# Optimization experiments

Hardware: AMD Instinct MI355X
Metric: run time of the kernel (lower is better)

## Reference

```python
import jax, jax.numpy as jnp
import numpy as np

B, L, K, D = 1024, 8, 16, 64
_KSCALE = 1.0 / np.sqrt(K * D)  # keep channel roughly norm-preserving over layers


def setup_inputs() -> dict:
    key = jax.random.key(0)
    k1, k2, k3, k4 = jax.random.split(key, 4)
    state_re = jax.random.normal(k1, (B, D, D), dtype=jnp.float32)
    state_im = jax.random.normal(k2, (B, D, D), dtype=jnp.float32)
    kraus_re = jax.random.normal(k3, (L, K, D, D), dtype=jnp.float32) * _KSCALE
    kraus_im = jax.random.normal(k4, (L, K, D, D), dtype=jnp.float32) * _KSCALE
    return {"state_re": state_re, "state_im": state_im,
            "kraus_re": kraus_re, "kraus_im": kraus_im}


def reference(state_re, state_im, kraus_re, kraus_im):
    # rho: [B, d, d] complex density matrices; kraus: [L, K, d, d]
    rho = (state_re + 1j * state_im).astype(jnp.complex64)
    kraus = (kraus_re + 1j * kraus_im).astype(jnp.complex64)

    def layer_step(rho, Kl):
        # Kl: [K, d, d]. output_state = sum_k  K_k @ rho @ K_k^dagger
        tmp = jnp.einsum('kij,bjl->kbil', Kl, rho)            # K_k @ rho
        rho_new = jnp.einsum('kbil,kml->bim', tmp, Kl.conj())  # (...) @ K_k^dagger, summed over k
        return rho_new, None

    rho, _ = jax.lax.scan(layer_step, rho, kraus)
    # return real/imag stacked as float32: [2, B, d, d]
    return jnp.stack([rho.real, rho.imag])
```

## Files before the change

kernel.cpp:

```cpp
#include <hip/hip_runtime.h>
#include <hip/hip_fp16.h>

#define D 64
#define NKR 16
#define NB 1024
#define NL 8
#define LSTR 72

typedef __attribute__((ext_vector_type(8))) _Float16 half8;
typedef __attribute__((ext_vector_type(4))) float f32x4;
typedef __attribute__((ext_vector_type(4))) int i32x4;

static __device__ __forceinline__ half8 neg8(half8 x) {
    i32x4 u = __builtin_bit_cast(i32x4, x);
    u = u ^ (int)0x80008000;
    return __builtin_bit_cast(half8, u);
}

union Pack4 { _Float16 h[4]; uint2 u; };

__global__ void kconv_kernel(const float* __restrict__ re, const float* __restrict__ im,
                             _Float16* __restrict__ out) {
    int plane = blockIdx.y;
    int idx = blockIdx.x * blockDim.x + threadIdx.x;
    const float* src = plane ? im : re;
    float4 v = ((const float4*)src)[idx];
    int e = idx * 4;
    int lk = e >> 12;
    int rem = e & 4095;
    Pack4 p;
    p.h[0] = (_Float16)v.x; p.h[1] = (_Float16)v.y;
    p.h[2] = (_Float16)v.z; p.h[3] = (_Float16)v.w;
    *(uint2*)(out + ((size_t)lk * 2 + plane) * 4096 + rem) = p.u;
}

__global__ void sconv_kernel(const float* __restrict__ re, const float* __restrict__ im,
                             _Float16* __restrict__ out) {
    __shared__ float tile[64][65];
    int b = blockIdx.x;
    int t = threadIdx.x;
    for (int plane = 0; plane < 2; ++plane) {
        const float* src = (plane ? im : re) + (size_t)b * 4096;
        __syncthreads();
        #pragma unroll
        for (int i = 0; i < 16; ++i) {
            int e = t + 256 * i;
            tile[e >> 6][e & 63] = src[e];
        }
        __syncthreads();
        _Float16* o = out + ((size_t)b * 2 + plane) * 4096;
        #pragma unroll
        for (int i = 0; i < 16; ++i) {
            int e = t + 256 * i;
            o[e] = (_Float16)tile[e & 63][e >> 6];
        }
    }
}

__global__ __launch_bounds__(256, 4) void layer_kernel(
    const _Float16* __restrict__ rho_in,
    _Float16* __restrict__ rho_out,
    float* __restrict__ final_out,
    const _Float16* __restrict__ kraus,
    int last)
{
    __shared__ __align__(16) _Float16 Klds[2][D][LSTR];
    __shared__ __align__(16) _Float16 Trow[2][D][LSTR];

    const int b    = blockIdx.x;
    const int t    = threadIdx.x;
    const int wv   = t >> 6;
    const int lane = t & 63;
    const int quad = lane >> 4;
    const int l15  = lane & 15;

    half8 a1re[2], a1im[2], a1imn[2];
    {
        const _Float16* rb = rho_in + (size_t)b * 2 * D * D;
        const int row = 16 * wv + l15;
        #pragma unroll
        for (int c = 0; c < 2; ++c) {
            const int col = 32 * c + 8 * quad;
            a1re[c]  = *(const half8*)(rb + row * D + col);
            a1im[c]  = *(const half8*)(rb + D * D + row * D + col);
            a1imn[c] = neg8(a1im[c]);
        }
    }

    f32x4 accRe[4] = {{0,0,0,0},{0,0,0,0},{0,0,0,0},{0,0,0,0}};
    f32x4 accIm[4] = {{0,0,0,0},{0,0,0,0},{0,0,0,0},{0,0,0,0}};

    #pragma unroll 1
    for (int k = 0; k < NKR; ++k) {
        const uint4* kg = (const uint4*)(kraus + (size_t)k * 2 * D * D);
        #pragma unroll
        for (int r = 0; r < 4; ++r) {
            int idx = t + 256 * r;
            int e0  = idx * 8;
            int plane = e0 >> 12;
            int rem   = e0 & 4095;
            int row = rem >> 6, col = rem & 63;
            *(uint4*)&Klds[plane][row][col] = kg[idx];
        }
        __syncthreads();

        #pragma unroll
        for (int ti = 0; ti < 4; ++ti) {
            f32x4 dre = {0,0,0,0}, dim = {0,0,0,0};
            #pragma unroll
            for (int c = 0; c < 2; ++c) {
                half8 bre = *(const half8*)&Klds[0][16 * ti + l15][32 * c + 8 * quad];
                half8 bim = *(const half8*)&Klds[1][16 * ti + l15][32 * c + 8 * quad];
                dre = __builtin_amdgcn_mfma_f32_16x16x32_f16(a1re[c],  bre, dre, 0, 0, 0);
                dre = __builtin_amdgcn_mfma_f32_16x16x32_f16(a1imn[c], bim, dre, 0, 0, 0);
                dim = __builtin_amdgcn_mfma_f32_16x16x32_f16(a1re[c],  bim, dim, 0, 0, 0);
                dim = __builtin_amdgcn_mfma_f32_16x16x32_f16(a1im[c],  bre, dim, 0, 0, 0);
            }
            const int i  = 16 * ti + l15;
            const int l0 = 16 * wv + 4 * quad;
            Pack4 pr, pi;
            #pragma unroll
            for (int r = 0; r < 4; ++r) { pr.h[r] = (_Float16)dre[r]; pi.h[r] = (_Float16)dim[r]; }
            *(uint2*)&Trow[0][i][l0] = pr.u;
            *(uint2*)&Trow[1][i][l0] = pi.u;
        }
        __syncthreads();

        #pragma unroll
        for (int c = 0; c < 2; ++c) {
            half8 are  = *(const half8*)&Trow[0][16 * wv + l15][32 * c + 8 * quad];
            half8 aim  = *(const half8*)&Trow[1][16 * wv + l15][32 * c + 8 * quad];
            half8 aren = neg8(are);
            #pragma unroll
            for (int tm = 0; tm < 4; ++tm) {
                half8 bre = *(const half8*)&Klds[0][16 * tm + l15][32 * c + 8 * quad];
                half8 bim = *(const half8*)&Klds[1][16 * tm + l15][32 * c + 8 * quad];
                accRe[tm] = __builtin_amdgcn_mfma_f32_16x16x32_f16(are,  bre, accRe[tm], 0, 0, 0);
                accRe[tm] = __builtin_amdgcn_mfma_f32_16x16x32_f16(aim,  bim, accRe[tm], 0, 0, 0);
                accIm[tm] = __builtin_amdgcn_mfma_f32_16x16x32_f16(aim,  bre, accIm[tm], 0, 0, 0);
                accIm[tm] = __builtin_amdgcn_mfma_f32_16x16x32_f16(aren, bim, accIm[tm], 0, 0, 0);
            }
        }
        __syncthreads();
    }

    if (!last) {
        _Float16* ob = rho_out + (size_t)b * 2 * D * D;
        const int i0 = 16 * wv + 4 * quad;
        #pragma unroll
        for (int tm = 0; tm < 4; ++tm) {
            const int m = 16 * tm + l15;
            Pack4 pr, pi;
            #pragma unroll
            for (int r = 0; r < 4; ++r) { pr.h[r] = (_Float16)accRe[tm][r]; pi.h[r] = (_Float16)accIm[tm][r]; }
            *(uint2*)(ob + m * D + i0)         = pr.u;
            *(uint2*)(ob + D * D + m * D + i0) = pi.u;
        }
    } else {
        float* o0 = final_out + (size_t)b * 4096;
        float* o1 = final_out + (size_t)(NB + b) * 4096;
        #pragma unroll
        for (int tm = 0; tm < 4; ++tm) {
            const int m = 16 * tm + l15;
            #pragma unroll
            for (int r = 0; r < 4; ++r) {
                const int i = 16 * wv + 4 * quad + r;
                o0[i * D + m] = accRe[tm][r];
                o1[i * D + m] = accIm[tm][r];
            }
        }
    }
}

extern "C" void kernel_launch(void* const* d_in, const int* in_sizes, int n_in,
                              void* d_out, int out_size, void* d_ws, size_t ws_size,
                              hipStream_t stream) {
    const float* state_re = (const float*)d_in[0];
    const float* state_im = (const float*)d_in[1];
    const float* kraus_re = (const float*)d_in[2];
    const float* kraus_im = (const float*)d_in[3];

    _Float16* kraus_h = (_Float16*)d_ws;
    _Float16* bufA = (_Float16*)d_out;
    _Float16* bufB = (_Float16*)((char*)d_out + (size_t)NB * 2 * D * D * sizeof(_Float16));
    float* fout = (float*)d_out;

    kconv_kernel<<<dim3(512, 2), 256, 0, stream>>>(kraus_re, kraus_im, kraus_h);
    sconv_kernel<<<NB, 256, 0, stream>>>(state_re, state_im, bufA);

    for (int l = 0; l < NL; ++l) {
        const _Float16* in = (l & 1) ? bufB : bufA;
        _Float16* out      = (l & 1) ? bufA : bufB;
        layer_kernel<<<NB, 256, 0, stream>>>(in, out, fout,
                                             kraus_h + (size_t)l * NKR * 2 * D * D,
                                             (l == NL - 1) ? 1 : 0);
    }
}
```

Baseline: 623.7 us.

## Switch layer kernel to 32x32x16 MFMA with 2x2 wave tiling

Replaces the 16x16x32 MFMA tiling, where each wave owned a 16-row strip, with 32x32x16 MFMA tiles. The four waves now form a 2x2 grid of 32x32 output blocks. Each wave issues fewer, larger MFMA instructions and reads less operand data from LDS per FLOP, with the Kraus and intermediate-matrix fragments shared across larger tiles. In exchange it uses larger accumulator vectors and a different writeback layout, which raises register pressure.

```diff
diff --git a/kernel.cpp b/kernel.cpp
--- a/kernel.cpp
+++ b/kernel.cpp
@@ -8,7 +8,7 @@
 #define LSTR 72
 
 typedef __attribute__((ext_vector_type(8))) _Float16 half8;
-typedef __attribute__((ext_vector_type(4))) float f32x4;
+typedef __attribute__((ext_vector_type(16))) float f32x16;
 typedef __attribute__((ext_vector_type(4))) int i32x4;
 
 static __device__ __forceinline__ half8 neg8(half8 x) {
@@ -71,24 +71,26 @@
     const int t    = threadIdx.x;
     const int wv   = t >> 6;
     const int lane = t & 63;
-    const int quad = lane >> 4;
-    const int l15  = lane & 15;
-
-    half8 a1re[2], a1im[2], a1imn[2];
+    const int l31  = lane & 31;
+    const int hl   = lane >> 5;
+    const int wr   = wv >> 1;
+    const int wc   = wv & 1;
+
+    half8 a1re[4], a1im[4];
     {
         const _Float16* rb = rho_in + (size_t)b * 2 * D * D;
-        const int row = 16 * wv + l15;
-        #pragma unroll
-        for (int c = 0; c < 2; ++c) {
-            const int col = 32 * c + 8 * quad;
-            a1re[c]  = *(const half8*)(rb + row * D + col);
-            a1im[c]  = *(const half8*)(rb + D * D + row * D + col);
-            a1imn[c] = neg8(a1im[c]);
-        }
-    }
-
-    f32x4 accRe[4] = {{0,0,0,0},{0,0,0,0},{0,0,0,0},{0,0,0,0}};
-    f32x4 accIm[4] = {{0,0,0,0},{0,0,0,0},{0,0,0,0},{0,0,0,0}};
+        const int row = 32 * wr + l31;
+        #pragma unroll
+        for (int ks = 0; ks < 4; ++ks) {
+            const int col = 16 * ks + 8 * hl;
+            a1re[ks] = *(const half8*)(rb + row * D + col);
+            a1im[ks] = *(const half8*)(rb + D * D + row * D + col);
+        }
+    }
+
+    f32x16 accRe, accIm;
+    #pragma unroll
+    for (int i = 0; i < 16; ++i) { accRe[i] = 0.f; accIm[i] = 0.f; }
 
     #pragma unroll 1
     for (int k = 0; k < NKR; ++k) {
@@ -99,74 +101,83 @@
             int e0  = idx * 8;
             int plane = e0 >> 12;
             int rem   = e0 & 4095;
-            int row = rem >> 6, col = rem & 63;
-            *(uint4*)&Klds[plane][row][col] = kg[idx];
-        }
-        __syncthreads();
-
-        #pragma unroll
-        for (int ti = 0; ti < 4; ++ti) {
-            f32x4 dre = {0,0,0,0}, dim = {0,0,0,0};
+            *(uint4*)&Klds[plane][rem >> 6][rem & 63] = kg[idx];
+        }
+        __syncthreads();
+
+        f32x16 dre, dim;
+        #pragma unroll
+        for (int i = 0; i < 16; ++i) { dre[i] = 0.f; dim[i] = 0.f; }
+        #pragma unroll
+        for (int ks = 0; ks < 4; ++ks) {
+            const int jcol = 16 * ks + 8 * hl;
+            half8 bre  = *(const half8*)&Klds[0][32 * wc + l31][jcol];
+            half8 bim  = *(const half8*)&Klds[1][32 * wc + l31][jcol];
+            half8 bimn = neg8(bim);
+            dre = __builtin_amdgcn_mfma_f32_32x32x16_f16(a1re[ks], bre,  dre, 0, 0, 0);
+            dre = __builtin_amdgcn_mfma_f32_32x32x16_f16(a1im[ks], bimn, dre, 0, 0, 0);
+            dim = __builtin_amdgcn_mfma_f32_32x32x16_f16(a1re[ks], bim,  dim, 0, 0, 0);
+            dim = __builtin_amdgcn_mfma_f32_32x32x16_f16(a1im[ks], bre,  dim, 0, 0, 0);
+        }
+        {
+            const int i = 32 * wc + l31;
             #pragma unroll
-            for (int c = 0; c < 2; ++c) {
-                half8 bre = *(const half8*)&Klds[0][16 * ti + l15][32 * c + 8 * quad];
-                half8 bim = *(const half8*)&Klds[1][16 * ti + l15][32 * c + 8 * quad];
-                dre = __builtin_amdgcn_mfma_f32_16x16x32_f16(a1re[c],  bre, dre, 0, 0, 0);
-                dre = __builtin_amdgcn_mfma_f32_16x16x32_f16(a1imn[c], bim, dre, 0, 0, 0);
-                dim = __builtin_amdgcn_mfma_f32_16x16x32_f16(a1re[c],  bim, dim, 0, 0, 0);
-                dim = __builtin_amdgcn_mfma_f32_16x16x32_f16(a1im[c],  bre, dim, 0, 0, 0);
+            for (int g = 0; g < 4; ++g) {
+                Pack4 pr, pi;
+                #pragma unroll
+                for (int j = 0; j < 4; ++j) {
+                    pr.h[j] = (_Float16)dre[4 * g + j];
+                    pi.h[j] = (_Float16)dim[4 * g + j];
+                }
+                const int l0 = 32 * wr + 8 * g + 4 * hl;
+                *(uint2*)&Trow[0][i][l0] = pr.u;
+                *(uint2*)&Trow[1][i][l0] = pi.u;
             }
-            const int i  = 16 * ti + l15;
-            const int l0 = 16 * wv + 4 * quad;
+        }
+        __syncthreads();
+
+        #pragma unroll
+        for (int ks = 0; ks < 4; ++ks) {
+            const int lcol = 16 * ks + 8 * hl;
+            half8 are  = *(const half8*)&Trow[0][32 * wr + l31][lcol];
+            half8 aim  = *(const half8*)&Trow[1][32 * wr + l31][lcol];
+            half8 bre  = *(const half8*)&Klds[0][32 * wc + l31][lcol];
+            half8 bim  = *(const half8*)&Klds[1][32 * wc + l31][lcol];
+            half8 bimn = neg8(bim);
+            accRe = __builtin_amdgcn_mfma_f32_32x32x16_f16(are, bre,  accRe, 0, 0, 0);
+            accRe = __builtin_amdgcn_mfma_f32_32x32x16_f16(aim, bim,  accRe, 0, 0, 0);
+            accIm = __builtin_amdgcn_mfma_f32_32x32x16_f16(aim, bre,  accIm, 0, 0, 0);
+            accIm = __builtin_amdgcn_mfma_f32_32x32x16_f16(are, bimn, accIm, 0, 0, 0);
+        }
+        __syncthreads();
+    }
+
+    if (!last) {
+        _Float16* ob = rho_out + (size_t)b * 2 * D * D;
+        const int m = 32 * wc + l31;
+        #pragma unroll
+        for (int g = 0; g < 4; ++g) {
             Pack4 pr, pi;
             #pragma unroll
-            for (int r = 0; r < 4; ++r) { pr.h[r] = (_Float16)dre[r]; pi.h[r] = (_Float16)dim[r]; }
-            *(uint2*)&Trow[0][i][l0] = pr.u;
-            *(uint2*)&Trow[1][i][l0] = pi.u;
-        }
-        __syncthreads();
-
-        #pragma unroll
-        for (int c = 0; c < 2; ++c) {
-            half8 are  = *(const half8*)&Trow[0][16 * wv + l15][32 * c + 8 * quad];
-            half8 aim  = *(const half8*)&Trow[1][16 * wv + l15][32 * c + 8 * quad];
-            half8 aren = neg8(are);
-            #pragma unroll
-            for (int tm = 0; tm < 4; ++tm) {
-                half8 bre = *(const half8*)&Klds[0][16 * tm + l15][32 * c + 8 * quad];
-                half8 bim = *(const half8*)&Klds[1][16 * tm + l15][32 * c + 8 * quad];
-                accRe[tm] = __builtin_amdgcn_mfma_f32_16x16x32_f16(are,  bre, accRe[tm], 0, 0, 0);
-                accRe[tm] = __builtin_amdgcn_mfma_f32_16x16x32_f16(aim,  bim, accRe[tm], 0, 0, 0);
-                accIm[tm] = __builtin_amdgcn_mfma_f32_16x16x32_f16(aim,  bre, accIm[tm], 0, 0, 0);
-                accIm[tm] = __builtin_amdgcn_mfma_f32_16x16x32_f16(aren, bim, accIm[tm], 0, 0, 0);
+            for (int j = 0; j < 4; ++j) {
+                pr.h[j] = (_Float16)accRe[4 * g + j];
+                pi.h[j] = (_Float16)accIm[4 * g + j];
             }
-        }
-        __syncthreads();
-    }
-
-    if (!last) {
-        _Float16* ob = rho_out + (size_t)b * 2 * D * D;
-        const int i0 = 16 * wv + 4 * quad;
-        #pragma unroll
-        for (int tm = 0; tm < 4; ++tm) {
-            const int m = 16 * tm + l15;
-            Pack4 pr, pi;
-            #pragma unroll
-            for (int r = 0; r < 4; ++r) { pr.h[r] = (_Float16)accRe[tm][r]; pi.h[r] = (_Float16)accIm[tm][r]; }
+            const int i0 = 32 * wr + 8 * g + 4 * hl;
             *(uint2*)(ob + m * D + i0)         = pr.u;
             *(uint2*)(ob + D * D + m * D + i0) = pi.u;
         }
     } else {
         float* o0 = final_out + (size_t)b * 4096;
         float* o1 = final_out + (size_t)(NB + b) * 4096;
-        #pragma unroll
-        for (int tm = 0; tm < 4; ++tm) {
-            const int m = 16 * tm + l15;
+        const int m = 32 * wc + l31;
+        #pragma unroll
+        for (int g = 0; g < 4; ++g) {
             #pragma unroll
-            for (int r = 0; r < 4; ++r) {
-                const int i = 16 * wv + 4 * quad + r;
-                o0[i * D + m] = accRe[tm][r];
-                o1[i * D + m] = accIm[tm][r];
+            for (int j = 0; j < 4; ++j) {
+                const int i = 32 * wr + 8 * g + 4 * hl + j;
+                o0[i * D + m] = accRe[4 * g + j];
+                o1[i * D + m] = accIm[4 * g + j];
             }
         }
     }
```

After: 612.3 us. Within noise of the previous version (-1.8%).
